# Optimization experiments

Hardware: AMD Instinct MI355X
Metric: run time of the kernel (lower is better)

## Reference

```python
import jax, jax.numpy as jnp
import numpy as np

MUL_IN = 32      # multiplicity of input 0e irrep (input channels)
MUL_OUT = 32     # multiplicity of each output irrep
NUM_RB = 8       # num_radial_basis
DIAMETER = 5.0
STEPS = (1.0, 1.0, 1.0)
GRID = 32
BATCH = 2
OUT_DIM = MUL_OUT * (1 + 3 + 5)  # 32x0e + 32x1o + 32x2e = 288


def _sus(x):
    # smooth unit step used by e3nn's 'smooth_finite' basis
    return jnp.where(x > 0.0, jnp.exp(-1.0 / jnp.where(x > 0.0, x, 1.0)), 0.0)


def _soft_one_hot(x, start, end, number):
    # e3nn.soft_one_hot_linspace, basis='smooth_finite', start_zero=end_zero=True
    values = jnp.linspace(start, end, number + 2)
    step = values[1] - values[0]
    values = values[1:-1]
    d = (x[..., None] - values) / step
    return 1.14136 * jnp.exp(2.0) * _sus(d + 1.0) * _sus(1.0 - d)


def _lattice():
    r = DIAMETER / 2
    axes = []
    for st in STEPS:
        s = int(np.floor(r / st))
        axes.append(jnp.arange(-s, s + 1.0, dtype=jnp.float32) * st)
    return jnp.stack(jnp.meshgrid(*axes, indexing='ij'), axis=-1)  # [X,Y,Z,3]


def _sph(lattice):
    # e3nn real spherical harmonics (component normalization, normalize=True),
    # e3nn axis/order convention: l=1 -> (y, z, x)
    n = jnp.linalg.norm(lattice, axis=-1, keepdims=True)
    u = lattice / jnp.where(n == 0.0, 1.0, n)
    x, y, z = u[..., 0], u[..., 1], u[..., 2]
    y0 = jnp.ones_like(x)[..., None]
    y1 = jnp.sqrt(3.0) * jnp.stack([y, z, x], axis=-1)
    y2 = jnp.stack([
        jnp.sqrt(15.0) * x * y,
        jnp.sqrt(15.0) * y * z,
        (jnp.sqrt(5.0) / 2.0) * (2.0 * z**2 - x**2 - y**2),
        jnp.sqrt(15.0) * x * z,
        (jnp.sqrt(15.0) / 2.0) * (x**2 - y**2),
    ], axis=-1)
    return [y0, y1, y2]


def _kernel(w0, w1, w2, w_lin):
    lat = _lattice()
    nvox = lat.shape[0] * lat.shape[1] * lat.shape[2]
    emb = _soft_one_hot(jnp.linalg.norm(lat, axis=-1), 0.0, DIAMETER / 2, NUM_RB)
    ys = _sph(lat)
    fan = jnp.sqrt(jnp.asarray(MUL_IN, emb.dtype))  # fully-connected TP path norm
    blocks = []
    for w, y in zip((w0, w1, w2), ys):
        # radial weights per (in-mul u, out-mul v): [X,Y,Z,u,v]
        W = jnp.einsum('xyzk,kuv->xyzuv', emb, w) / nvox
        # scalar-input TP path 0e x l -> l reduces to outer product with Y_lm
        blk = jnp.einsum('xyzuv,xyzm->xyzuvm', W, y) / fan
        blocks.append(blk.reshape(blk.shape[:4] + (-1,)))  # flatten (v, m)
    k = jnp.concatenate(blocks, axis=-1)  # [X,Y,Z,MUL_IN,OUT_DIM]
    # self-connection (FunctionalLinear) replaces the center tap; only 0e->0e path
    center = jnp.concatenate(
        [w_lin / fan, jnp.zeros((MUL_IN, MUL_OUT * (3 + 5)), k.dtype)], axis=-1)
    cx, cy, cz = k.shape[0] // 2, k.shape[1] // 2, k.shape[2] // 2
    return k.at[cx, cy, cz].set(center)


def setup_inputs() -> dict:
    key = jax.random.key(0)
    ks = jax.random.split(key, 5)
    return {
        'x': jax.random.normal(ks[0], (BATCH, GRID, GRID, GRID, MUL_IN), jnp.float32),
        'w0': jax.random.normal(ks[1], (NUM_RB, MUL_IN, MUL_OUT), jnp.float32),
        'w1': jax.random.normal(ks[2], (NUM_RB, MUL_IN, MUL_OUT), jnp.float32),
        'w2': jax.random.normal(ks[3], (NUM_RB, MUL_IN, MUL_OUT), jnp.float32),
        'w_lin': jax.random.normal(ks[4], (MUL_IN, MUL_OUT), jnp.float32),
    }


def reference(x, w0, w1, w2, w_lin):
    k = _kernel(w0, w1, w2, w_lin)  # [5,5,5,32,288]
    return jax.lax.conv_general_dilated(
        x, k, window_strides=(1, 1, 1), padding='SAME',
        dimension_numbers=('NXYZC', 'XYZIO', 'NXYZC'))
```

## Files before the change

### kernel.cpp

```cpp
#include <hip/hip_runtime.h>

typedef __bf16 bf16x8 __attribute__((ext_vector_type(8)));
typedef float f32x4 __attribute__((ext_vector_type(4)));

#define KT_BYTES 2304000
#define NS 18432
#define NV 87

__device__ __forceinline__ unsigned short f2bf(float f) {
    unsigned int u = __builtin_bit_cast(unsigned int, f);
    unsigned int r = (u + 0x7fffu + ((u >> 16) & 1u)) >> 16;
    return (unsigned short)r;
}

__device__ __forceinline__ float sus(float x) {
    return x > 0.0f ? expf(-1.0f / x) : 0.0f;
}

struct VoxTab { int kt[NV]; int xb[NV]; };
constexpr VoxTab mk_tab() {
    VoxTab t{};
    int n = 0;
    for (int dx = 0; dx < 5; dx++)
        for (int dy = 0; dy < 5; dy++)
            for (int dz = 0; dz < 5; dz++) {
                int a = dx - 2, b = dy - 2, c = dz - 2;
                if (a * a + b * b + c * c <= 6) {
                    t.kt[n] = (dx * 25 + dy * 5 + dz) * NS;
                    t.xb[n] = ((dx * 36 + dy) * 36 + dz) * 32;
                    n++;
                }
            }
    for (; n < NV; n++) { t.kt[n] = 0; t.xb[n] = 0; }
    return t;
}
__constant__ VoxTab TAB = mk_tab();

__global__ __launch_bounds__(512) void build_kt(const float* __restrict__ w0,
                                                const float* __restrict__ w1,
                                                const float* __restrict__ w2,
                                                const float* __restrict__ wlin,
                                                unsigned short* __restrict__ kt) {
    __shared__ float lw[24576];
    const int tid = threadIdx.x;
    {
        const float4* s0 = (const float4*)w0;
        const float4* s1 = (const float4*)w1;
        const float4* s2 = (const float4*)w2;
        for (int u = tid; u < 6144; u += 512) {
            int wsel = u >> 11, r = u & 2047;
            float4 v = (wsel == 0 ? s0[r] : (wsel == 1 ? s1[r] : s2[r]));
            ((float4*)lw)[u] = v;
        }
    }
    __syncthreads();

    const int v = blockIdx.x;
    const int dx = v / 25, dy = (v / 5) % 5, dz = v % 5;
    const float lx = (float)(dx - 2), ly = (float)(dy - 2), lz = (float)(dz - 2);
    const float nr = sqrtf(lx * lx + ly * ly + lz * lz);

    float emb[8];
    const float tt = nr * (9.0f / 2.5f);
    const float C = 1.14136f * expf(2.0f);
    #pragma unroll
    for (int j = 1; j <= 8; j++) {
        float d = tt - (float)j;
        emb[j - 1] = C * sus(d + 1.0f) * sus(1.0f - d);
    }

    float ux = 0.f, uy = 0.f, uz = 0.f;
    if (nr > 0.0f) { ux = lx / nr; uy = ly / nr; uz = lz / nr; }
    float Y[9];
    const float s3 = 1.7320508075688772f, s15 = 3.872983346207417f;
    Y[0] = 1.0f;
    Y[1] = s3 * uy; Y[2] = s3 * uz; Y[3] = s3 * ux;
    Y[4] = s15 * ux * uy;
    Y[5] = s15 * uy * uz;
    Y[6] = 1.1180339887498949f * (2.0f * uz * uz - ux * ux - uy * uy);
    Y[7] = s15 * ux * uz;
    Y[8] = 0.5f * s15 * (ux * ux - uy * uy);

    const float rfan = 0.17677669529663687f;

    for (int e = tid; e < 9216; e += 512) {
        const int ci = e / 288, o = e % 288;
        int wsel, co, yi;
        if (o < 32)       { wsel = 0; co = o; yi = 0; }
        else if (o < 128) { int t = o - 32;  wsel = 1; co = t / 3; yi = 1 + t % 3; }
        else              { int t = o - 128; wsel = 2; co = t / 5; yi = 4 + t % 5; }
        const float* w = lw + wsel * 8192;
        float s = 0.0f;
        #pragma unroll
        for (int k = 0; k < 8; k++) s += emb[k] * w[k * 1024 + ci * 32 + co];
        float val = s * (1.0f / 125.0f) * Y[yi] * rfan;
        if (v == 62) val = (o < 32) ? wlin[ci * 32 + o] * rfan : 0.0f;
        int r = o * 64 + ci * 2;
        int rs = r ^ (((r >> 7) & 7) << 4);
        kt[v * 9216 + (rs >> 1)] = f2bf(val);
    }
}

__global__ void pad_x2(const float* __restrict__ x, unsigned short* __restrict__ xb) {
    int u = blockIdx.x * blockDim.x + threadIdx.x;
    if (u >= 373248) return;
    const int ci8 = u & 3;
    int t = u >> 2;
    const int pz = t % 36; t /= 36;
    const int py = t % 36; t /= 36;
    const int px = t % 36; const int nn = t / 36;
    const int gx = px - 2, gy = py - 2, gz = pz - 2;
    uint4 ov = {0u, 0u, 0u, 0u};
    if ((unsigned)gx < 32u && (unsigned)gy < 32u && (unsigned)gz < 32u) {
        const float* src = x + ((((size_t)nn * 32 + gx) * 32 + gy) * 32 + gz) * 32 + ci8 * 8;
        float4 f0 = ((const float4*)src)[0];
        float4 f1 = ((const float4*)src)[1];
        ov.x = (unsigned)f2bf(f0.x) | ((unsigned)f2bf(f0.y) << 16);
        ov.y = (unsigned)f2bf(f0.z) | ((unsigned)f2bf(f0.w) << 16);
        ov.z = (unsigned)f2bf(f1.x) | ((unsigned)f2bf(f1.y) << 16);
        ov.w = (unsigned)f2bf(f1.z) | ((unsigned)f2bf(f1.w) << 16);
    }
    ((uint4*)xb)[u] = ov;
}

__global__ __launch_bounds__(512, 2) void conv_mfma(const unsigned short* __restrict__ xb,
                                                    const unsigned short* __restrict__ kt,
                                                    float* __restrict__ out) {
    __shared__ __align__(16) char lds[4 * NS];
    const int tid = threadIdx.x;
    const int lane = tid & 63;
    const int wv = tid >> 6;
    const int l15 = lane & 15, l16 = lane >> 4;
    const int wm = wv & 3, wn = wv >> 2;
    const int o0 = wn * 144;

    const int b = blockIdx.x;
    const int sw = (b & 7) * 32 + (b >> 3);
    const int nn = sw >> 7;
    const int X0 = 2 * ((sw >> 3) & 15);
    const int Y0 = 4 * (sw & 7);

    const unsigned short* xbase = xb + (size_t)nn * 1492992;

    int aoff[4];
    #pragma unroll
    for (int s = 0; s < 4; s++) {
        int xw = X0 + (wm >> 1);
        int yw = Y0 + (wm & 1) * 2 + (s >> 1);
        int zb = (s & 1) * 16 + l15;
        aoff[s] = ((xw * 36 + yw) * 36 + zb) * 32 + l16 * 8;
    }
    int boff[9];
    #pragma unroll
    for (int nt = 0; nt < 9; nt++) {
        int a = (o0 + nt * 16 + l15) * 64 + l16 * 16;
        boff[nt] = a ^ (((a >> 7) & 7) << 4);
    }

    auto stageB = [&](int ktByte, int slot) {
        const char* src = (const char*)kt + ktByte + wv * 2304;
        char* dst = lds + slot * NS + wv * 2304;
        __builtin_amdgcn_global_load_lds(
            (const __attribute__((address_space(1))) void*)(src + lane * 16),
            (__attribute__((address_space(3))) void*)dst, 16, 0, 0);
        __builtin_amdgcn_global_load_lds(
            (const __attribute__((address_space(1))) void*)(src + 1024 + lane * 16),
            (__attribute__((address_space(3))) void*)(dst + 1024), 16, 0, 0);
        __builtin_amdgcn_global_load_lds(
            (const __attribute__((address_space(1))) void*)(src + 2048 + lane * 4),
            (__attribute__((address_space(3))) void*)(dst + 2048), 4, 0, 0);
    };

    bf16x8 A0[4], A1[4];
    f32x4 acc[4][9];
    #pragma unroll
    for (int i = 0; i < 4; i++)
        #pragma unroll
        for (int j = 0; j < 9; j++)
            acc[i][j] = (f32x4){0.f, 0.f, 0.f, 0.f};

    auto loadA = [&](bf16x8* A, int xoff) {
        #pragma unroll
        for (int s = 0; s < 4; s++)
            A[s] = *(const bf16x8*)(xbase + aoff[s] + xoff);
    };

    auto compute = [&](bf16x8* A, int slot) {
        #pragma unroll
        for (int nt = 0; nt < 9; nt++) {
            bf16x8 bfr = *(const bf16x8*)(lds + slot * NS + boff[nt]);
            #pragma unroll
            for (int s = 0; s < 4; s++)
                acc[s][nt] = __builtin_amdgcn_mfma_f32_16x16x32_bf16(A[s], bfr, acc[s][nt], 0, 0, 0);
        }
    };

    #define PHASE(CUR, NXT, K)                                          \
        asm volatile("s_waitcnt vmcnt(7)" ::: "memory");                \
        __builtin_amdgcn_sched_barrier(0);                              \
        __builtin_amdgcn_s_barrier();                                   \
        __builtin_amdgcn_sched_barrier(0);                              \
        stageB(TAB.kt[(K) + 3], ((K) + 3) & 3);                         \
        loadA(NXT, TAB.xb[(K) + 1]);                                    \
        compute(CUR, (K) & 3);

    stageB(TAB.kt[0], 0);
    stageB(TAB.kt[1], 1);
    stageB(TAB.kt[2], 2);
    loadA(A0, TAB.xb[0]);

    #pragma unroll 1
    for (int g = 0; g < 21; g++) {
        const int k = g * 4;
        PHASE(A0, A1, k + 0)
        PHASE(A1, A0, k + 1)
        PHASE(A0, A1, k + 2)
        PHASE(A1, A0, k + 3)
    }
    #undef PHASE

    #pragma unroll
    for (int s = 0; s < 4; s++) {
        const int x = X0 + (wm >> 1);
        const int y = Y0 + (wm & 1) * 2 + (s >> 1);
        #pragma unroll
        for (int r = 0; r < 4; r++) {
            int z = (s & 1) * 16 + l16 * 4 + r;
            size_t base = ((((size_t)nn * 32 + x) * 32 + y) * 32 + z) * 288 + o0 + l15;
            #pragma unroll
            for (int nt = 0; nt < 9; nt++)
                out[base + nt * 16] = acc[s][nt][r];
        }
    }
}

extern "C" void kernel_launch(void* const* d_in, const int* in_sizes, int n_in,
                              void* d_out, int out_size, void* d_ws, size_t ws_size,
                              hipStream_t stream) {
    const float* x    = (const float*)d_in[0];
    const float* w0   = (const float*)d_in[1];
    const float* w1   = (const float*)d_in[2];
    const float* w2   = (const float*)d_in[3];
    const float* wlin = (const float*)d_in[4];
    unsigned short* kt = (unsigned short*)d_ws;
    unsigned short* xb = (unsigned short*)((char*)d_ws + KT_BYTES);
    float* out = (float*)d_out;

    hipLaunchKernelGGL(build_kt, dim3(125), dim3(512), 0, stream, w0, w1, w2, wlin, kt);
    hipLaunchKernelGGL(pad_x2, dim3(1458), dim3(256), 0, stream, x, xb);
    hipLaunchKernelGGL(conv_mfma, dim3(256), dim3(512), 0, stream, xb, kt, out);
}
```

Before: 130.8 us.

## Drop LDS staging of kernel taps; load B fragments directly from global

```diff
diff --git a/kernel.cpp b/kernel.cpp
--- a/kernel.cpp
+++ b/kernel.cpp
@@ -5,7 +5,7 @@
 
 #define KT_BYTES 2304000
 #define NS 18432
-#define NV 87
+#define NACT 81
 
 __device__ __forceinline__ unsigned short f2bf(float f) {
     unsigned int u = __builtin_bit_cast(unsigned int, f);
@@ -17,7 +17,7 @@
     return x > 0.0f ? expf(-1.0f / x) : 0.0f;
 }
 
-struct VoxTab { int kt[NV]; int xb[NV]; };
+struct VoxTab { int kt[NACT]; int xb[NACT]; };
 constexpr VoxTab mk_tab() {
     VoxTab t{};
     int n = 0;
@@ -31,7 +31,6 @@
                     n++;
                 }
             }
-    for (; n < NV; n++) { t.kt[n] = 0; t.xb[n] = 0; }
     return t;
 }
 __constant__ VoxTab TAB = mk_tab();
@@ -95,9 +94,7 @@
         for (int k = 0; k < 8; k++) s += emb[k] * w[k * 1024 + ci * 32 + co];
         float val = s * (1.0f / 125.0f) * Y[yi] * rfan;
         if (v == 62) val = (o < 32) ? wlin[ci * 32 + o] * rfan : 0.0f;
-        int r = o * 64 + ci * 2;
-        int rs = r ^ (((r >> 7) & 7) << 4);
-        kt[v * 9216 + (rs >> 1)] = f2bf(val);
+        kt[v * 9216 + o * 32 + ci] = f2bf(val);
     }
 }
 
@@ -126,7 +123,6 @@
 __global__ __launch_bounds__(512, 2) void conv_mfma(const unsigned short* __restrict__ xb,
                                                     const unsigned short* __restrict__ kt,
                                                     float* __restrict__ out) {
-    __shared__ __align__(16) char lds[4 * NS];
     const int tid = threadIdx.x;
     const int lane = tid & 63;
     const int wv = tid >> 6;
@@ -150,28 +146,8 @@
         int zb = (s & 1) * 16 + l15;
         aoff[s] = ((xw * 36 + yw) * 36 + zb) * 32 + l16 * 8;
     }
-    int boff[9];
-    #pragma unroll
-    for (int nt = 0; nt < 9; nt++) {
-        int a = (o0 + nt * 16 + l15) * 64 + l16 * 16;
-        boff[nt] = a ^ (((a >> 7) & 7) << 4);
-    }
-
-    auto stageB = [&](int ktByte, int slot) {
-        const char* src = (const char*)kt + ktByte + wv * 2304;
-        char* dst = lds + slot * NS + wv * 2304;
-        __builtin_amdgcn_global_load_lds(
-            (const __attribute__((address_space(1))) void*)(src + lane * 16),
-            (__attribute__((address_space(3))) void*)dst, 16, 0, 0);
-        __builtin_amdgcn_global_load_lds(
-            (const __attribute__((address_space(1))) void*)(src + 1024 + lane * 16),
-            (__attribute__((address_space(3))) void*)(dst + 1024), 16, 0, 0);
-        __builtin_amdgcn_global_load_lds(
-            (const __attribute__((address_space(1))) void*)(src + 2048 + lane * 4),
-            (__attribute__((address_space(3))) void*)(dst + 2048), 4, 0, 0);
-    };
-
-    bf16x8 A0[4], A1[4];
+    const char* kbase = (const char*)kt + (o0 + l15) * 64 + l16 * 16;
+
     f32x4 acc[4][9];
     #pragma unroll
     for (int i = 0; i < 4; i++)
@@ -179,45 +155,27 @@
         for (int j = 0; j < 9; j++)
             acc[i][j] = (f32x4){0.f, 0.f, 0.f, 0.f};
 
-    auto loadA = [&](bf16x8* A, int xoff) {
-        #pragma unroll
-        for (int s = 0; s < 4; s++)
-            A[s] = *(const bf16x8*)(xbase + aoff[s] + xoff);
-    };
-
-    auto compute = [&](bf16x8* A, int slot) {
-        #pragma unroll
-        for (int nt = 0; nt < 9; nt++) {
-            bf16x8 bfr = *(const bf16x8*)(lds + slot * NS + boff[nt]);
+    #pragma unroll 1
+    for (int g = 0; g < 27; g++) {
+        #pragma unroll
+        for (int q = 0; q < 3; q++) {
+            const int k = g * 3 + q;
+            const unsigned short* ax = xbase + TAB.xb[k];
+            const char* kb = kbase + TAB.kt[k];
+            bf16x8 A[4];
             #pragma unroll
             for (int s = 0; s < 4; s++)
-                acc[s][nt] = __builtin_amdgcn_mfma_f32_16x16x32_bf16(A[s], bfr, acc[s][nt], 0, 0, 0);
+                A[s] = *(const bf16x8*)(ax + aoff[s]);
+            #pragma unroll
+            for (int nt = 0; nt < 9; nt++) {
+                bf16x8 B = *(const bf16x8*)(kb + nt * 1024);
+                #pragma unroll
+                for (int s = 0; s < 4; s++)
+                    acc[s][nt] = __builtin_amdgcn_mfma_f32_16x16x32_bf16(A[s], B, acc[s][nt], 0, 0, 0);
+            }
         }
-    };
-
-    #define PHASE(CUR, NXT, K)                                          \
-        asm volatile("s_waitcnt vmcnt(7)" ::: "memory");                \
-        __builtin_amdgcn_sched_barrier(0);                              \
-        __builtin_amdgcn_s_barrier();                                   \
-        __builtin_amdgcn_sched_barrier(0);                              \
-        stageB(TAB.kt[(K) + 3], ((K) + 3) & 3);                         \
-        loadA(NXT, TAB.xb[(K) + 1]);                                    \
-        compute(CUR, (K) & 3);
-
-    stageB(TAB.kt[0], 0);
-    stageB(TAB.kt[1], 1);
-    stageB(TAB.kt[2], 2);
-    loadA(A0, TAB.xb[0]);
-
-    #pragma unroll 1
-    for (int g = 0; g < 21; g++) {
-        const int k = g * 4;
-        PHASE(A0, A1, k + 0)
-        PHASE(A1, A0, k + 1)
-        PHASE(A0, A1, k + 2)
-        PHASE(A1, A0, k + 3)
-    }
-    #undef PHASE
+        __builtin_amdgcn_s_barrier();
+    }
 
     #pragma unroll
     for (int s = 0; s < 4; s++) {
```

Result: slower. 177.9 us (+36.0%).

## Halve per-block output tile to double grid and raise occupancy

Applied to the files above, without the earlier changes.

```diff
diff --git a/kernel.cpp b/kernel.cpp
--- a/kernel.cpp
+++ b/kernel.cpp
@@ -5,7 +5,7 @@
 
 #define KT_BYTES 2304000
 #define NS 18432
-#define NV 87
+#define NV 84
 
 __device__ __forceinline__ unsigned short f2bf(float f) {
     unsigned int u = __builtin_bit_cast(unsigned int, f);
@@ -123,7 +123,7 @@
     ((uint4*)xb)[u] = ov;
 }
 
-__global__ __launch_bounds__(512, 2) void conv_mfma(const unsigned short* __restrict__ xb,
+__global__ __launch_bounds__(512, 4) void conv_mfma(const unsigned short* __restrict__ xb,
                                                     const unsigned short* __restrict__ kt,
                                                     float* __restrict__ out) {
     __shared__ __align__(16) char lds[4 * NS];
@@ -135,27 +135,18 @@
     const int o0 = wn * 144;
 
     const int b = blockIdx.x;
-    const int sw = (b & 7) * 32 + (b >> 3);
-    const int nn = sw >> 7;
-    const int X0 = 2 * ((sw >> 3) & 15);
-    const int Y0 = 4 * (sw & 7);
+    const int sw = (b & 7) * 64 + (b >> 3);
+    const int nn = sw >> 8;
+    const int X0 = 2 * ((sw >> 4) & 15);
+    const int Y0 = 2 * (sw & 15);
 
     const unsigned short* xbase = xb + (size_t)nn * 1492992;
 
-    int aoff[4];
-    #pragma unroll
-    for (int s = 0; s < 4; s++) {
-        int xw = X0 + (wm >> 1);
-        int yw = Y0 + (wm & 1) * 2 + (s >> 1);
-        int zb = (s & 1) * 16 + l15;
-        aoff[s] = ((xw * 36 + yw) * 36 + zb) * 32 + l16 * 8;
-    }
-    int boff[9];
-    #pragma unroll
-    for (int nt = 0; nt < 9; nt++) {
-        int a = (o0 + nt * 16 + l15) * 64 + l16 * 16;
-        boff[nt] = a ^ (((a >> 7) & 7) << 4);
-    }
+    const int axy = ((X0 + (wm >> 1)) * 36 + (Y0 + (wm & 1))) * 36;
+    const int aoff0 = (axy + l15) * 32 + l16 * 8;
+
+    int bbase = (o0 + l15) * 64 + l16 * 16;
+    bbase ^= ((bbase >> 7) & 7) << 4;
 
     auto stageB = [&](int ktByte, int slot) {
         const char* src = (const char*)kt + ktByte + wv * 2304;
@@ -171,37 +162,37 @@
             (__attribute__((address_space(3))) void*)(dst + 2048), 4, 0, 0);
     };
 
-    bf16x8 A0[4], A1[4];
-    f32x4 acc[4][9];
+    bf16x8 A0[2], A1[2];
+    f32x4 acc[2][9];
     #pragma unroll
-    for (int i = 0; i < 4; i++)
+    for (int i = 0; i < 2; i++)
         #pragma unroll
         for (int j = 0; j < 9; j++)
             acc[i][j] = (f32x4){0.f, 0.f, 0.f, 0.f};
 
     auto loadA = [&](bf16x8* A, int xoff) {
-        #pragma unroll
-        for (int s = 0; s < 4; s++)
-            A[s] = *(const bf16x8*)(xbase + aoff[s] + xoff);
+        const unsigned short* p = xbase + aoff0 + xoff;
+        A[0] = *(const bf16x8*)p;
+        A[1] = *(const bf16x8*)(p + 512);
     };
 
     auto compute = [&](bf16x8* A, int slot) {
+        const char* bp = lds + slot * NS + bbase;
         #pragma unroll
         for (int nt = 0; nt < 9; nt++) {
-            bf16x8 bfr = *(const bf16x8*)(lds + slot * NS + boff[nt]);
-            #pragma unroll
-            for (int s = 0; s < 4; s++)
-                acc[s][nt] = __builtin_amdgcn_mfma_f32_16x16x32_bf16(A[s], bfr, acc[s][nt], 0, 0, 0);
+            bf16x8 B = *(const bf16x8*)(bp + nt * 1024);
+            acc[0][nt] = __builtin_amdgcn_mfma_f32_16x16x32_bf16(A[0], B, acc[0][nt], 0, 0, 0);
+            acc[1][nt] = __builtin_amdgcn_mfma_f32_16x16x32_bf16(A[1], B, acc[1][nt], 0, 0, 0);
         }
     };
 
     #define PHASE(CUR, NXT, K)                                          \
-        asm volatile("s_waitcnt vmcnt(7)" ::: "memory");                \
+        asm volatile("s_waitcnt vmcnt(3)" ::: "memory");                \
         __builtin_amdgcn_sched_barrier(0);                              \
         __builtin_amdgcn_s_barrier();                                   \
         __builtin_amdgcn_sched_barrier(0);                              \
+        loadA(NXT, TAB.xb[(K) + 1]);                                    \
         stageB(TAB.kt[(K) + 3], ((K) + 3) & 3);                         \
-        loadA(NXT, TAB.xb[(K) + 1]);                                    \
         compute(CUR, (K) & 3);
 
     stageB(TAB.kt[0], 0);
@@ -210,22 +201,21 @@
     loadA(A0, TAB.xb[0]);
 
     #pragma unroll 1
-    for (int g = 0; g < 21; g++) {
-        const int k = g * 4;
+    for (int g = 0; g < 40; g++) {
+        const int k = g * 2;
         PHASE(A0, A1, k + 0)
         PHASE(A1, A0, k + 1)
-        PHASE(A0, A1, k + 2)
-        PHASE(A1, A0, k + 3)
-    }
+    }
+    PHASE(A0, A1, 80)
     #undef PHASE
 
+    const int x = X0 + (wm >> 1);
+    const int y = Y0 + (wm & 1);
     #pragma unroll
-    for (int s = 0; s < 4; s++) {
-        const int x = X0 + (wm >> 1);
-        const int y = Y0 + (wm & 1) * 2 + (s >> 1);
+    for (int s = 0; s < 2; s++) {
         #pragma unroll
         for (int r = 0; r < 4; r++) {
-            int z = (s & 1) * 16 + l16 * 4 + r;
+            int z = s * 16 + l16 * 4 + r;
             size_t base = ((((size_t)nn * 32 + x) * 32 + y) * 32 + z) * 288 + o0 + l15;
             #pragma unroll
             for (int nt = 0; nt < 9; nt++)
@@ -248,5 +238,5 @@
 
     hipLaunchKernelGGL(build_kt, dim3(125), dim3(512), 0, stream, w0, w1, w2, wlin, kt);
     hipLaunchKernelGGL(pad_x2, dim3(1458), dim3(256), 0, stream, x, xb);
-    hipLaunchKernelGGL(conv_mfma, dim3(256), dim3(512), 0, stream, xb, kt, out);
-}
+    hipLaunchKernelGGL(conv_mfma, dim3(512), dim3(512), 0, stream, xb, kt, out);
+}
```

Result: faster. 110.2 us (-15.7%).

## Split conv tile across waves by output channel and drop block barrier

Applied to the files above, without the earlier changes.

```diff
diff --git a/kernel.cpp b/kernel.cpp
--- a/kernel.cpp
+++ b/kernel.cpp
@@ -5,7 +5,7 @@
 
 #define KT_BYTES 2304000
 #define NS 18432
-#define NV 87
+#define NVT 85
 
 __device__ __forceinline__ unsigned short f2bf(float f) {
     unsigned int u = __builtin_bit_cast(unsigned int, f);
@@ -17,7 +17,7 @@
     return x > 0.0f ? expf(-1.0f / x) : 0.0f;
 }
 
-struct VoxTab { int kt[NV]; int xb[NV]; };
+struct VoxTab { int kt[NVT]; int xb[NVT]; };
 constexpr VoxTab mk_tab() {
     VoxTab t{};
     int n = 0;
@@ -31,7 +31,7 @@
                     n++;
                 }
             }
-    for (; n < NV; n++) { t.kt[n] = 0; t.xb[n] = 0; }
+    for (; n < NVT; n++) { t.kt[n] = 0; t.xb[n] = 0; }
     return t;
 }
 __constant__ VoxTab TAB = mk_tab();
@@ -123,7 +123,7 @@
     ((uint4*)xb)[u] = ov;
 }
 
-__global__ __launch_bounds__(512, 2) void conv_mfma(const unsigned short* __restrict__ xb,
+__global__ __launch_bounds__(384, 3) void conv_mfma(const unsigned short* __restrict__ xb,
                                                     const unsigned short* __restrict__ kt,
                                                     float* __restrict__ out) {
     __shared__ __align__(16) char lds[4 * NS];
@@ -131,52 +131,45 @@
     const int lane = tid & 63;
     const int wv = tid >> 6;
     const int l15 = lane & 15, l16 = lane >> 4;
-    const int wm = wv & 3, wn = wv >> 2;
-    const int o0 = wn * 144;
+    const int o0 = wv * 48;
 
     const int b = blockIdx.x;
-    const int sw = (b & 7) * 32 + (b >> 3);
-    const int nn = sw >> 7;
-    const int X0 = 2 * ((sw >> 3) & 15);
-    const int Y0 = 4 * (sw & 7);
+    const int sw = (b & 7) * 128 + (b >> 3);
+    const int nn = sw >> 9;
+    const int rem = sw & 511;
+    const int X0 = rem >> 4;
+    const int Y0 = (rem & 15) * 2;
 
     const unsigned short* xbase = xb + (size_t)nn * 1492992;
 
     int aoff[4];
     #pragma unroll
-    for (int s = 0; s < 4; s++) {
-        int xw = X0 + (wm >> 1);
-        int yw = Y0 + (wm & 1) * 2 + (s >> 1);
-        int zb = (s & 1) * 16 + l15;
-        aoff[s] = ((xw * 36 + yw) * 36 + zb) * 32 + l16 * 8;
-    }
-    int boff[9];
-    #pragma unroll
-    for (int nt = 0; nt < 9; nt++) {
-        int a = (o0 + nt * 16 + l15) * 64 + l16 * 16;
-        boff[nt] = a ^ (((a >> 7) & 7) << 4);
-    }
+    for (int s = 0; s < 4; s++)
+        aoff[s] = ((X0 * 36 + Y0 + (s >> 1)) * 36 + (s & 1) * 16 + l15) * 32 + l16 * 8;
+
+    int bbase = (o0 + l15) * 64 + l16 * 16;
+    bbase ^= ((bbase >> 7) & 7) << 4;
 
     auto stageB = [&](int ktByte, int slot) {
-        const char* src = (const char*)kt + ktByte + wv * 2304;
-        char* dst = lds + slot * NS + wv * 2304;
+        const char* src = (const char*)kt + ktByte + wv * 3072 + lane * 16;
+        char* dst = lds + slot * NS + wv * 3072 + lane * 16;
         __builtin_amdgcn_global_load_lds(
-            (const __attribute__((address_space(1))) void*)(src + lane * 16),
+            (const __attribute__((address_space(1))) void*)src,
             (__attribute__((address_space(3))) void*)dst, 16, 0, 0);
         __builtin_amdgcn_global_load_lds(
-            (const __attribute__((address_space(1))) void*)(src + 1024 + lane * 16),
+            (const __attribute__((address_space(1))) void*)(src + 1024),
             (__attribute__((address_space(3))) void*)(dst + 1024), 16, 0, 0);
         __builtin_amdgcn_global_load_lds(
-            (const __attribute__((address_space(1))) void*)(src + 2048 + lane * 4),
-            (__attribute__((address_space(3))) void*)(dst + 2048), 4, 0, 0);
+            (const __attribute__((address_space(1))) void*)(src + 2048),
+            (__attribute__((address_space(3))) void*)(dst + 2048), 16, 0, 0);
     };
 
     bf16x8 A0[4], A1[4];
-    f32x4 acc[4][9];
+    f32x4 acc[4][3];
     #pragma unroll
     for (int i = 0; i < 4; i++)
         #pragma unroll
-        for (int j = 0; j < 9; j++)
+        for (int j = 0; j < 3; j++)
             acc[i][j] = (f32x4){0.f, 0.f, 0.f, 0.f};
 
     auto loadA = [&](bf16x8* A, int xoff) {
@@ -186,49 +179,45 @@
     };
 
     auto compute = [&](bf16x8* A, int slot) {
-        #pragma unroll
-        for (int nt = 0; nt < 9; nt++) {
-            bf16x8 bfr = *(const bf16x8*)(lds + slot * NS + boff[nt]);
+        const char* bp = lds + slot * NS + bbase;
+        #pragma unroll
+        for (int nt = 0; nt < 3; nt++) {
+            bf16x8 B = *(const bf16x8*)(bp + nt * 1024);
             #pragma unroll
             for (int s = 0; s < 4; s++)
-                acc[s][nt] = __builtin_amdgcn_mfma_f32_16x16x32_bf16(A[s], bfr, acc[s][nt], 0, 0, 0);
+                acc[s][nt] = __builtin_amdgcn_mfma_f32_16x16x32_bf16(A[s], B, acc[s][nt], 0, 0, 0);
         }
     };
 
     #define PHASE(CUR, NXT, K)                                          \
-        asm volatile("s_waitcnt vmcnt(7)" ::: "memory");                \
+        asm volatile("s_waitcnt vmcnt(3)" ::: "memory");                \
         __builtin_amdgcn_sched_barrier(0);                              \
-        __builtin_amdgcn_s_barrier();                                   \
-        __builtin_amdgcn_sched_barrier(0);                              \
+        loadA(NXT, TAB.xb[(K) + 1]);                                    \
         stageB(TAB.kt[(K) + 3], ((K) + 3) & 3);                         \
-        loadA(NXT, TAB.xb[(K) + 1]);                                    \
         compute(CUR, (K) & 3);
 
+    loadA(A0, TAB.xb[0]);
     stageB(TAB.kt[0], 0);
     stageB(TAB.kt[1], 1);
     stageB(TAB.kt[2], 2);
-    loadA(A0, TAB.xb[0]);
 
     #pragma unroll 1
-    for (int g = 0; g < 21; g++) {
-        const int k = g * 4;
+    for (int g = 0; g < 41; g++) {
+        const int k = 2 * g;
         PHASE(A0, A1, k + 0)
         PHASE(A1, A0, k + 1)
-        PHASE(A0, A1, k + 2)
-        PHASE(A1, A0, k + 3)
     }
     #undef PHASE
 
     #pragma unroll
     for (int s = 0; s < 4; s++) {
-        const int x = X0 + (wm >> 1);
-        const int y = Y0 + (wm & 1) * 2 + (s >> 1);
+        const int y = Y0 + (s >> 1);
         #pragma unroll
         for (int r = 0; r < 4; r++) {
             int z = (s & 1) * 16 + l16 * 4 + r;
-            size_t base = ((((size_t)nn * 32 + x) * 32 + y) * 32 + z) * 288 + o0 + l15;
+            size_t base = ((((size_t)nn * 32 + X0) * 32 + y) * 32 + z) * 288 + o0 + l15;
             #pragma unroll
-            for (int nt = 0; nt < 9; nt++)
+            for (int nt = 0; nt < 3; nt++)
                 out[base + nt * 16] = acc[s][nt][r];
         }
     }
@@ -248,5 +237,5 @@
 
     hipLaunchKernelGGL(build_kt, dim3(125), dim3(512), 0, stream, w0, w1, w2, wlin, kt);
     hipLaunchKernelGGL(pad_x2, dim3(1458), dim3(256), 0, stream, x, xb);
-    hipLaunchKernelGGL(conv_mfma, dim3(256), dim3(512), 0, stream, xb, kt, out);
-}
+    hipLaunchKernelGGL(conv_mfma, dim3(1024), dim3(384), 0, stream, xb, kt, out);
+}
```

Result: slower. 215.0 us (+64.4%).
